# Kernel optimization log

Measured on AMD Instinct MI355X. Metric: run time of the kernel, lower is better.

## Reference

```python
import jax, jax.numpy as jnp
import numpy as np

N_NODES = 50000
N_EDGES = 800000
B, S, D = 512, 200, 128
H = 8


def setup_inputs() -> dict:
    key = jax.random.key(0)
    ks = iter(jax.random.split(key, 64))
    def nrm(shape, scale=0.05):
        return jax.random.normal(next(ks), shape, dtype=jnp.float32) * scale
    inp = {
        'hist_seq': jax.random.randint(next(ks), (B, S), 0, N_NODES, dtype=jnp.int32),
        'hist_answers': jax.random.randint(next(ks), (B, S), 0, 2, dtype=jnp.int32),
        'new_seq': jax.random.randint(next(ks), (B, S), 0, N_NODES, dtype=jnp.int32),
        'edge_index': jax.random.randint(next(ks), (2, N_EDGES), 0, N_NODES, dtype=jnp.int32),
        'node_x': nrm((N_NODES, D)),
        'gcn_w0': nrm((D, D)), 'gcn_b0': jnp.zeros((D,), jnp.float32),
        'gcn_w1': nrm((D, D)), 'gcn_b1': jnp.zeros((D,), jnp.float32),
        'gcn_w2': nrm((D, D)), 'gcn_b2': jnp.zeros((D,), jnp.float32),
        'ln0_g': jnp.ones((D,), jnp.float32), 'ln0_b': jnp.zeros((D,), jnp.float32),
        'ln1_g': jnp.ones((D,), jnp.float32), 'ln1_b': jnp.zeros((D,), jnp.float32),
        'ln2_g': jnp.ones((D,), jnp.float32), 'ln2_b': jnp.zeros((D,), jnp.float32),
        'ln3_g': jnp.ones((D,), jnp.float32), 'ln3_b': jnp.zeros((D,), jnp.float32),
        'corr_emb': nrm((2, D)),
        'lin0_w': nrm((2 * D, D)), 'lin0_b': jnp.zeros((D,), jnp.float32),
        'lin1_w': nrm((D, D)), 'lin2_w': nrm((D, D)), 'lin3_w': nrm((D, D)),
        'lin4_w': nrm((D, 1)), 'lin4_b': jnp.zeros((1,), jnp.float32),
        'pos_emb': nrm((S, D)),
        'mha_wq': nrm((D, D)), 'mha_bq': jnp.zeros((D,), jnp.float32),
        'mha_wk': nrm((D, D)), 'mha_bk': jnp.zeros((D,), jnp.float32),
        'mha_wv': nrm((D, D)), 'mha_bv': jnp.zeros((D,), jnp.float32),
        'mha_wo': nrm((D, D)), 'mha_bo': jnp.zeros((D,), jnp.float32),
        'ffn0_w': nrm((D, D)), 'ffn0_b': jnp.zeros((D,), jnp.float32),
        'ffn1_w': nrm((D, D)), 'ffn1_b': jnp.zeros((D,), jnp.float32),
    }
    return inp


def _layer_norm(x, g, b, eps=1e-5):
    m = jnp.mean(x, axis=-1, keepdims=True)
    v = jnp.var(x, axis=-1, keepdims=True)
    return (x - m) * jax.lax.rsqrt(v + eps) * g + b


def _forward(hist_seq, hist_answers, new_seq, edge_index, node_x,
             gcn_w0, gcn_b0, gcn_w1, gcn_b1, gcn_w2, gcn_b2,
             ln0_g, ln0_b, ln1_g, ln1_b, ln2_g, ln2_b, ln3_g, ln3_b,
             corr_emb, lin0_w, lin0_b, lin1_w, lin2_w, lin3_w, lin4_w, lin4_b,
             pos_emb, mha_wq, mha_bq, mha_wk, mha_bk, mha_wv, mha_bv,
             mha_wo, mha_bo, ffn0_w, ffn0_b, ffn1_w, ffn1_b):
    N = node_x.shape[0]
    loop = jnp.arange(N, dtype=edge_index.dtype)
    src = jnp.concatenate([edge_index[0], loop])  # self-loops as in PyG GCNConv
    dst = jnp.concatenate([edge_index[1], loop])
    deg = jax.ops.segment_sum(jnp.ones_like(dst, dtype=node_x.dtype), dst, num_segments=N)
    dis = jax.lax.rsqrt(deg)  # deg >= 1 (self-loops)
    norm = dis[src] * dis[dst]

    def gcn(x, W, b):
        xw = x @ W
        return jax.ops.segment_sum(norm[:, None] * xw[src], dst, num_segments=N) + b

    x = _layer_norm(jax.nn.relu(gcn(node_x, gcn_w0, gcn_b0)), ln0_g, ln0_b)
    x = _layer_norm(jax.nn.relu(gcn(x, gcn_w1, gcn_b1)), ln1_g, ln1_b)
    x = jax.nn.relu(gcn(x, gcn_w2, gcn_b2))  # last GCN layer: no LN

    # vectorized embedding gathers (the original's per-element loops)
    hist_emb = x[hist_seq]            # [B,S,D]
    new_emb = x[new_seq]              # [B,S,D]
    ans_emb = corr_emb[hist_answers]  # [B,S,D]

    inter = jnp.concatenate([hist_emb, ans_emb], axis=-1) @ lin0_w + lin0_b
    inter = inter + pos_emb[None]  # [B,S,D]

    v = inter @ lin1_w
    k = inter @ lin2_w
    q = new_emb @ lin3_w

    b_, s_, d_ = q.shape
    dh = d_ // H
    qh = (q @ mha_wq + mha_bq).reshape(b_, s_, H, dh)
    kh = (k @ mha_wk + mha_bk).reshape(b_, s_, H, dh)
    vh = (v @ mha_wv + mha_bv).reshape(b_, s_, H, dh)
    scores = jnp.einsum('bqhd,bkhd->bhqk', qh, kh) / jnp.sqrt(jnp.asarray(dh, q.dtype))
    causal = jnp.triu(jnp.ones((s_, s_), dtype=bool), k=1)
    scores = jnp.where(causal[None, None], -jnp.inf, scores)
    attn = jax.nn.softmax(scores, axis=-1)
    ao = jnp.einsum('bhqk,bkhd->bqhd', attn, vh).reshape(b_, s_, d_)
    ao = ao @ mha_wo + mha_bo

    atn = _layer_norm(ao + q, ln2_g, ln2_b)
    ffn = jax.nn.relu(atn @ ffn0_w + ffn0_b) @ ffn1_w + ffn1_b
    out = _layer_norm(ffn + atn, ln3_g, ln3_b)
    pred = (out @ lin4_w + lin4_b)[..., 0]  # squeeze -> [B,S]
    return pred


def reference(hist_seq, hist_answers, new_seq, edge_index, node_x,
              gcn_w0, gcn_b0, gcn_w1, gcn_b1, gcn_w2, gcn_b2,
              ln0_g, ln0_b, ln1_g, ln1_b, ln2_g, ln2_b, ln3_g, ln3_b,
              corr_emb, lin0_w, lin0_b, lin1_w, lin2_w, lin3_w, lin4_w, lin4_b,
              pos_emb, mha_wq, mha_bq, mha_wk, mha_bk, mha_wv, mha_bv,
              mha_wo, mha_bo, ffn0_w, ffn0_b, ffn1_w, ffn1_b):
    return _forward(hist_seq, hist_answers, new_seq, edge_index, node_x,
                    gcn_w0, gcn_b0, gcn_w1, gcn_b1, gcn_w2, gcn_b2,
                    ln0_g, ln0_b, ln1_g, ln1_b, ln2_g, ln2_b, ln3_g, ln3_b,
                    corr_emb, lin0_w, lin0_b, lin1_w, lin2_w, lin3_w, lin4_w, lin4_b,
                    pos_emb, mha_wq, mha_bq, mha_wk, mha_bk, mha_wv, mha_bv,
                    mha_wo, mha_bo, ffn0_w, ffn0_b, ffn1_w, ffn1_b)
```

## Files before the change

### kernel.cpp

```cpp
#include <hip/hip_runtime.h>
#include <math.h>

#define N_NODES 50000
#define N_EDGES 800000
#define B_ 512
#define S_ 200
#define D_ 128
#define BS_ (B_*S_)

typedef unsigned short u16;
typedef unsigned int u32;
using bfrag = __attribute__((ext_vector_type(8))) short;
using f32x4 = __attribute__((ext_vector_type(4))) float;

__device__ __forceinline__ u16 f2bf(float f) {
  u32 u = __float_as_uint(f);
  u32 r = (u + 0x7fffu + ((u >> 16) & 1u)) >> 16;
  return (u16)r;
}
__device__ __forceinline__ float bf2f(u16 v) { return __uint_as_float(((u32)v) << 16); }
__device__ __forceinline__ float bflo(u32 v) { return __uint_as_float(v << 16); }
__device__ __forceinline__ float bfhi(u32 v) { return __uint_as_float(v & 0xffff0000u); }
__device__ __forceinline__ u32 pack2(float a, float b) {
  return (u32)f2bf(a) | ((u32)f2bf(b) << 16);
}
#define MFMA16(a, b, c) __builtin_amdgcn_mfma_f32_16x16x32_bf16((a), (b), (c), 0, 0, 0)

#define STAGE_W(Wsrc) \
  for (int i_ = threadIdx.x; i_ < 2048; i_ += 256) { \
    int c_ = i_ >> 4, kg_ = i_ & 15; \
    *(uint4*)(sW + c_ * 136 + kg_ * 8) = *(const uint4*)((Wsrc) + c_ * 128 + kg_ * 8); \
  }

__global__ void zero_i32_kernel(int* __restrict__ p, int n) {
  int i = blockIdx.x * 256 + threadIdx.x;
  if (i < n) p[i] = 0;
}

__global__ void f2bf8_kernel(const float* __restrict__ in, u16* __restrict__ out, int n8) {
  int i = blockIdx.x * 256 + threadIdx.x;
  if (i >= n8) return;
  float4 a = ((const float4*)in)[i * 2];
  float4 b = ((const float4*)in)[i * 2 + 1];
  uint4 o;
  o.x = pack2(a.x, a.y); o.y = pack2(a.z, a.w);
  o.z = pack2(b.x, b.y); o.w = pack2(b.z, b.w);
  ((uint4*)out)[i] = o;
}

__global__ __launch_bounds__(256) void wprep_kernel(
    const float* __restrict__ gcn_w0, const float* __restrict__ gcn_w1,
    const float* __restrict__ gcn_w2, const float* __restrict__ lin0_w,
    const float* __restrict__ lin3_w, const float* __restrict__ mha_wo,
    const float* __restrict__ ffn0_w, const float* __restrict__ ffn1_w,
    const float* __restrict__ lin1_w, const float* __restrict__ lin2_w,
    const float* __restrict__ mha_wq, const float* __restrict__ mha_wk,
    const float* __restrict__ mha_wv, const float* __restrict__ corr_emb,
    u16* __restrict__ g0T, u16* __restrict__ g1T, u16* __restrict__ g2T,
    u16* __restrict__ l0T, u16* __restrict__ l3T, u16* __restrict__ woT,
    u16* __restrict__ f0T, u16* __restrict__ f1T,
    u16* __restrict__ wqT, u16* __restrict__ wkT, u16* __restrict__ wvT,
    float* __restrict__ c01) {
  int bb = blockIdx.x;
  if (bb < 512) {
    const float* W; u16* D;
    switch (bb >> 6) {
      case 0: W = gcn_w0; D = g0T; break;
      case 1: W = gcn_w1; D = g1T; break;
      case 2: W = gcn_w2; D = g2T; break;
      case 3: W = lin0_w; D = l0T; break;
      case 4: W = lin3_w; D = l3T; break;
      case 5: W = mha_wo; D = woT; break;
      case 6: W = ffn0_w; D = f0T; break;
      default: W = ffn1_w; D = f1T; break;
    }
    int i = (bb & 63) * 256 + threadIdx.x;
    int k = i >> 7, c = i & 127;
    D[c * 128 + k] = f2bf(W[k * 128 + c]);
  } else if (bb < 704) {
    const float* X; const float* Y; u16* D;
    switch ((bb - 512) >> 6) {
      case 0: X = lin3_w; Y = mha_wq; D = wqT; break;
      case 1: X = lin2_w; Y = mha_wk; D = wkT; break;
      default: X = lin1_w; Y = mha_wv; D = wvT; break;
    }
    int i = ((bb - 512) & 63) * 256 + threadIdx.x;
    int k = i >> 7, c = i & 127;
    float acc = 0.f;
    for (int t = 0; t < 128; ++t) acc += X[k * 128 + t] * Y[t * 128 + c];
    D[c * 128 + k] = f2bf(acc);
  } else {
    int idx = threadIdx.x;
    int i = idx >> 7, j = idx & 127;
    float acc = 0.f;
    for (int t = 0; t < 128; ++t)
      acc += corr_emb[i * 128 + t] * lin0_w[128 * 128 + t * 128 + j];
    c01[idx] = acc;
  }
}

__global__ void pc_kernel(const float* __restrict__ lin0_b, const float* __restrict__ pos_emb,
                          const float* __restrict__ c01, float* __restrict__ pc) {
  int i = blockIdx.x * 256 + threadIdx.x;
  int c = i & 127, s = (i >> 7) % S_, a = i / (128 * S_);
  pc[i] = lin0_b[c] + pos_emb[s * 128 + c] + c01[a * 128 + c];
}

__global__ void hist_kernel(const int* __restrict__ dst, int* __restrict__ cnt, int E) {
  int e = blockIdx.x * 256 + threadIdx.x;
  if (e < E) atomicAdd(&cnt[dst[e]], 1);
}

__global__ __launch_bounds__(1024) void scanA_kernel(
    const int* __restrict__ cnt, int* __restrict__ locpref,
    int* __restrict__ btot, float* __restrict__ dis, int N) {
  __shared__ int wsum[16];
  int t = threadIdx.x, lane = t & 63, wid = t >> 6;
  int i = blockIdx.x * 1024 + t;
  int v = (i < N) ? cnt[i] : 0;
  if (i < N) dis[i] = rsqrtf(1.f + (float)v);
  int x = v;
  #pragma unroll
  for (int off = 1; off < 64; off <<= 1) {
    int y = __shfl_up(x, off);
    if (lane >= off) x += y;
  }
  if (lane == 63) wsum[wid] = x;
  __syncthreads();
  if (wid == 0 && lane < 16) {
    int s = wsum[lane];
    #pragma unroll
    for (int off = 1; off < 16; off <<= 1) {
      int y = __shfl_up(s, off);
      if (lane >= off) s += y;
    }
    wsum[lane] = s;
  }
  __syncthreads();
  int woff = (wid > 0) ? wsum[wid - 1] : 0;
  if (i < N) locpref[i] = woff + x - v;
  if (t == 1023) btot[blockIdx.x] = woff + x;
}

__global__ void scanB_kernel(const int* __restrict__ btot, int* __restrict__ boff, int nb) {
  int lane = threadIdx.x;
  int v = (lane < nb) ? btot[lane] : 0;
  int x = v;
  #pragma unroll
  for (int off = 1; off < 64; off <<= 1) {
    int y = __shfl_up(x, off);
    if (lane >= off) x += y;
  }
  if (lane < nb) boff[lane] = x - v;
}

__global__ void scanC_kernel(const int* __restrict__ locpref, const int* __restrict__ boff,
                             int* __restrict__ row_ptr, int* __restrict__ fill, int N) {
  int i = blockIdx.x * 256 + threadIdx.x;
  if (i < N) {
    int r = locpref[i] + boff[i >> 10];
    row_ptr[i] = r; fill[i] = r;
  }
  if (i == 0) row_ptr[N] = N_EDGES;
}

__global__ void scatter_kernel(const int* __restrict__ src, const int* __restrict__ dst,
                               int* __restrict__ fill, int* __restrict__ csr_src, int E) {
  int e = blockIdx.x * 256 + threadIdx.x;
  if (e >= E) return;
  int d = dst[e];
  int pos = atomicAdd(&fill[d], 1);
  csr_src[pos] = src[e];
}

__global__ __launch_bounds__(256) void gemm_bf16_kernel(
    const u16* __restrict__ A, const u16* __restrict__ wT,
    u16* __restrict__ C, int M) {
  __shared__ u16 ldsb[4][16 * 136];
  int t = threadIdx.x;
  int w = t >> 6, l = t & 63, lr = l & 15, lg = l >> 4;
  int r0 = blockIdx.x * 64 + w * 16;

  int row = r0 + lr;
  const u16* Arow = A + (size_t)(row < M ? row : 0) * 128;

  bfrag a[4];
  #pragma unroll
  for (int ks = 0; ks < 4; ++ks) a[ks] = *(const bfrag*)(Arow + ks * 32 + lg * 8);

  f32x4 acc[8];
  #pragma unroll
  for (int ct = 0; ct < 8; ++ct) acc[ct] = (f32x4){0.f, 0.f, 0.f, 0.f};
  #pragma unroll
  for (int ks = 0; ks < 4; ++ks)
    #pragma unroll
    for (int ct = 0; ct < 8; ++ct) {
      bfrag b = *(const bfrag*)(wT + (size_t)(ct * 16 + lr) * 128 + ks * 32 + lg * 8);
      acc[ct] = MFMA16(a[ks], b, acc[ct]);
    }
  #pragma unroll
  for (int ct = 0; ct < 8; ++ct)
    #pragma unroll
    for (int i = 0; i < 4; ++i)
      ldsb[w][(lg * 4 + i) * 136 + ct * 16 + lr] = f2bf(acc[ct][i]);
  #pragma unroll
  for (int j = 0; j < 4; ++j) {
    int c = j * 64 + l;
    int rw = c >> 4, ch = c & 15;
    int r = r0 + rw;
    if (r < M)
      *(uint4*)(C + (size_t)r * 128 + ch * 8) = *(const uint4*)&ldsb[w][rw * 136 + ch * 8];
  }
}

__global__ __launch_bounds__(256) void agg_kernel(
    const u16* __restrict__ xw, const float* __restrict__ dis,
    const int* __restrict__ row_ptr, const int* __restrict__ csr_src,
    const float* __restrict__ bias, const float* __restrict__ lng,
    const float* __restrict__ lnb, u16* __restrict__ out, int N, int doLN) {
  int t = threadIdx.x;
  int n = blockIdx.x * 4 + (t >> 6);
  if (n >= N) return;
  int l = t & 63, cg = l & 15, eg = l >> 4;
  float dn = dis[n];
  float acc[8] = {0.f, 0.f, 0.f, 0.f, 0.f, 0.f, 0.f, 0.f};
  if (eg == 0) {
    uint4 r = *(const uint4*)(xw + (size_t)n * 128 + cg * 8);
    float w = dn * dn;
    acc[0] += w * bflo(r.x); acc[1] += w * bfhi(r.x);
    acc[2] += w * bflo(r.y); acc[3] += w * bfhi(r.y);
    acc[4] += w * bflo(r.z); acc[5] += w * bfhi(r.z);
    acc[6] += w * bflo(r.w); acc[7] += w * bfhi(r.w);
  }
  int e1 = row_ptr[n + 1];
  int e = row_ptr[n] + eg;
  int sn = (e < e1) ? csr_src[e] : -1;
  while (sn >= 0) {
    int s = sn;
    e += 4;
    sn = (e < e1) ? csr_src[e] : -1;
    float w = dis[s] * dn;
    uint4 r = *(const uint4*)(xw + (size_t)s * 128 + cg * 8);
    acc[0] += w * bflo(r.x); acc[1] += w * bfhi(r.x);
    acc[2] += w * bflo(r.y); acc[3] += w * bfhi(r.y);
    acc[4] += w * bflo(r.z); acc[5] += w * bfhi(r.z);
    acc[6] += w * bflo(r.w); acc[7] += w * bfhi(r.w);
  }
  #pragma unroll
  for (int j = 0; j < 8; ++j) {
    acc[j] += __shfl_xor(acc[j], 16);
    acc[j] += __shfl_xor(acc[j], 32);
  }
  int c0 = cg * 8;
  #pragma unroll
  for (int j = 0; j < 8; ++j) acc[j] = fmaxf(acc[j] + bias[c0 + j], 0.f);
  if (doLN) {
    float s1 = 0.f, s2 = 0.f;
    #pragma unroll
    for (int j = 0; j < 8; ++j) { s1 += acc[j]; s2 += acc[j] * acc[j]; }
    #pragma unroll
    for (int off = 1; off < 16; off <<= 1) {
      s1 += __shfl_xor(s1, off);
      s2 += __shfl_xor(s2, off);
    }
    float mean = s1 * (1.f / 128.f);
    float var = s2 * (1.f / 128.f) - mean * mean;
    float inv = rsqrtf(var + 1e-5f);
    #pragma unroll
    for (int j = 0; j < 8; ++j)
      acc[j] = (acc[j] - mean) * inv * lng[c0 + j] + lnb[c0 + j];
  }
  if (eg == 0) {
    uint4 o;
    o.x = pack2(acc[0], acc[1]); o.y = pack2(acc[2], acc[3]);
    o.z = pack2(acc[4], acc[5]); o.w = pack2(acc[6], acc[7]);
    *(uint4*)(out + (size_t)n * 128 + cg * 8) = o;
  }
}

__global__ __launch_bounds__(256) void qkv_kernel(
    const u16* __restrict__ xa, const int* __restrict__ hist,
    const int* __restrict__ ans, const int* __restrict__ nseq,
    const u16* __restrict__ l0T, const float* __restrict__ pc,
    const u16* __restrict__ wkT, const float* __restrict__ bk,
    const u16* __restrict__ wvT, const float* __restrict__ bv,
    const u16* __restrict__ wqT, const float* __restrict__ bq,
    u16* __restrict__ khout, u16* __restrict__ vhout,
    u16* __restrict__ qhout, int nblk) {
  __shared__ u16 sW[128 * 136];
  __shared__ u16 ldsb[4][16 * 136];
  int bb = blockIdx.x;
  int t = threadIdx.x, w = t >> 6, l = t & 63, lr = l & 15, lg = l >> 4;
  f32x4 acc[8];

  if (bb < nblk) {
    int r0 = bb * 64 + w * 16;
    int arow = hist[r0 + lr];
    const u16* Arow = xa + (size_t)arow * 128;
    bfrag a[4];
    #pragma unroll
    for (int ks = 0; ks < 4; ++ks) a[ks] = *(const bfrag*)(Arow + ks * 32 + lg * 8);

    STAGE_W(l0T);
    __syncthreads();
    #pragma unroll
    for (int ct = 0; ct < 8; ++ct) acc[ct] = (f32x4){0.f, 0.f, 0.f, 0.f};
    #pragma unroll
    for (int ks = 0; ks < 4; ++ks)
      #pragma unroll
      for (int ct = 0; ct < 8; ++ct) {
        bfrag b = *(const bfrag*)(sW + (ct * 16 + lr) * 136 + ks * 32 + lg * 8);
        acc[ct] = MFMA16(a[ks], b, acc[ct]);
      }
    int pcoff[4];
    #pragma unroll
    for (int i = 0; i < 4; ++i) {
      int r = r0 + lg * 4 + i;
      pcoff[i] = (ans[r] * S_ + (r % S_)) * 128;
    }
    #pragma unroll
    for (int ct = 0; ct < 8; ++ct) {
      int col = ct * 16 + lr;
      #pragma unroll
      for (int i = 0; i < 4; ++i)
        ldsb[w][(lg * 4 + i) * 136 + col] = f2bf(acc[ct][i] + pc[pcoff[i] + col]);
    }
    bfrag a2[4];
    #pragma unroll
    for (int ks = 0; ks < 4; ++ks)
      a2[ks] = *(const bfrag*)(&ldsb[w][lr * 136 + ks * 32 + lg * 8]);
    __syncthreads();

    STAGE_W(wkT);
    __syncthreads();
    #pragma unroll
    for (int ct = 0; ct < 8; ++ct) acc[ct] = (f32x4){0.f, 0.f, 0.f, 0.f};
    #pragma unroll
    for (int ks = 0; ks < 4; ++ks)
      #pragma unroll
      for (int ct = 0; ct < 8; ++ct) {
        bfrag b = *(const bfrag*)(sW + (ct * 16 + lr) * 136 + ks * 32 + lg * 8);
        acc[ct] = MFMA16(a2[ks], b, acc[ct]);
      }
    #pragma unroll
    for (int ct = 0; ct < 8; ++ct)
      #pragma unroll
      for (int i = 0; i < 4; ++i)
        ldsb[w][(lg * 4 + i) * 136 + ct * 16 + lr] = f2bf(acc[ct][i] + bk[ct * 16 + lr]);
    #pragma unroll
    for (int j = 0; j < 4; ++j) {
      int c = j * 64 + l;
      int head = c >> 5, rw = (c >> 1) & 15, half = c & 1;
      *(uint4*)(khout + ((size_t)head * BS_ + r0 + rw) * 16 + half * 8) =
          *(const uint4*)&ldsb[w][rw * 136 + head * 16 + half * 8];
    }
    __syncthreads();

    STAGE_W(wvT);
    __syncthreads();
    #pragma unroll
    for (int ct = 0; ct < 8; ++ct) acc[ct] = (f32x4){0.f, 0.f, 0.f, 0.f};
    #pragma unroll
    for (int ks = 0; ks < 4; ++ks)
      #pragma unroll
      for (int ct = 0; ct < 8; ++ct) {
        bfrag b = *(const bfrag*)(sW + (ct * 16 + lr) * 136 + ks * 32 + lg * 8);
        acc[ct] = MFMA16(a2[ks], b, acc[ct]);
      }
    #pragma unroll
    for (int ct = 0; ct < 8; ++ct)
      #pragma unroll
      for (int i = 0; i < 4; ++i)
        ldsb[w][(lg * 4 + i) * 136 + ct * 16 + lr] = f2bf(acc[ct][i] + bv[ct * 16 + lr]);
    #pragma unroll
    for (int j = 0; j < 4; ++j) {
      int c = j * 64 + l;
      int head = c >> 5, rw = (c >> 1) & 15, half = c & 1;
      *(uint4*)(vhout + ((size_t)head * BS_ + r0 + rw) * 16 + half * 8) =
          *(const uint4*)&ldsb[w][rw * 136 + head * 16 + half * 8];
    }
  } else {
    int r0 = (bb - nblk) * 64 + w * 16;
    int arow = nseq[r0 + lr];
    const u16* Arow = xa + (size_t)arow * 128;
    bfrag a[4];
    #pragma unroll
    for (int ks = 0; ks < 4; ++ks) a[ks] = *(const bfrag*)(Arow + ks * 32 + lg * 8);

    STAGE_W(wqT);
    __syncthreads();
    #pragma unroll
    for (int ct = 0; ct < 8; ++ct) acc[ct] = (f32x4){0.f, 0.f, 0.f, 0.f};
    #pragma unroll
    for (int ks = 0; ks < 4; ++ks)
      #pragma unroll
      for (int ct = 0; ct < 8; ++ct) {
        bfrag b = *(const bfrag*)(sW + (ct * 16 + lr) * 136 + ks * 32 + lg * 8);
        acc[ct] = MFMA16(a[ks], b, acc[ct]);
      }
    #pragma unroll
    for (int ct = 0; ct < 8; ++ct)
      #pragma unroll
      for (int i = 0; i < 4; ++i)
        ldsb[w][(lg * 4 + i) * 136 + ct * 16 + lr] = f2bf(acc[ct][i] + bq[ct * 16 + lr]);
    #pragma unroll
    for (int j = 0; j < 4; ++j) {
      int c = j * 64 + l;
      int head = c >> 5, rw = (c >> 1) & 15, half = c & 1;
      *(uint4*)(qhout + ((size_t)head * BS_ + r0 + rw) * 16 + half * 8) =
          *(const uint4*)&ldsb[w][rw * 136 + head * 16 + half * 8];
    }
  }
}

__global__ __launch_bounds__(256) void attn_mfma_kernel(
    u16* qh_ao, const u16* __restrict__ kh, const u16* __restrict__ vh) {
  __shared__ u16 Kl[208 * 24];
  __shared__ u16 Vt[16 * 232];
  __shared__ u16 Pl[4 * 16 * 232];
  int b = blockIdx.x >> 3, h = blockIdx.x & 7;
  int t = threadIdx.x;
  size_t base = ((size_t)h * BS_ + (size_t)b * S_) * 16;

  for (int i = t; i < 208 * 2; i += 256) {
    int key = i >> 1, d = (i & 1) * 8;
    uint4 v = make_uint4(0, 0, 0, 0);
    if (key < S_) v = *(const uint4*)(kh + base + (size_t)key * 16 + d);
    *(uint4*)(Kl + key * 24 + d) = v;
  }
  for (int i = t; i < 16 * 232; i += 256) {
    int d = i / 232, key = i - d * 232;
    Vt[d * 232 + key] = (key < S_) ? vh[base + (size_t)key * 16 + d] : (u16)0;
  }
  for (int i = t; i < 4 * 16 * 232 / 2; i += 256) ((u32*)Pl)[i] = 0;
  __syncthreads();

  int w = t >> 6, l = t & 63, lr = l & 15, lg = l >> 4;
  u16* Pw = Pl + w * 16 * 232;
  const f32x4 zero4 = {0.f, 0.f, 0.f, 0.f};

  for (int qi = w; qi < 13; qi += 4) {
    bfrag aq = (bfrag){0, 0, 0, 0, 0, 0, 0, 0};
    int qrow = qi * 16 + lr;
    if (lg < 2 && qrow < S_)
      aq = *(const bfrag*)(qh_ao + base + (size_t)qrow * 16 + lg * 8);
    float rsum[4] = {0.f, 0.f, 0.f, 0.f};
    for (int kj = 0; kj <= qi; ++kj) {
      bfrag bk = (bfrag){0, 0, 0, 0, 0, 0, 0, 0};
      if (lg < 2) bk = *(const bfrag*)(Kl + (kj * 16 + lr) * 24 + lg * 8);
      f32x4 sc = MFMA16(aq, bk, zero4);
      #pragma unroll
      for (int i = 0; i < 4; ++i) {
        int q = qi * 16 + lg * 4 + i, key = kj * 16 + lr;
        float p = 0.f;
        if (key <= q && q < S_) p = __expf(sc[i] * 0.25f);
        rsum[i] += p;
        Pw[(lg * 4 + i) * 232 + key] = f2bf(p);
      }
    }
    #pragma unroll
    for (int i = 0; i < 4; ++i) {
      rsum[i] += __shfl_xor(rsum[i], 1);
      rsum[i] += __shfl_xor(rsum[i], 2);
      rsum[i] += __shfl_xor(rsum[i], 4);
      rsum[i] += __shfl_xor(rsum[i], 8);
    }
    f32x4 o = zero4;
    #pragma unroll
    for (int kt = 0; kt < 7; ++kt) {
      bfrag ap = *(const bfrag*)(Pw + lr * 232 + kt * 32 + lg * 8);
      bfrag bv = *(const bfrag*)(Vt + lr * 232 + kt * 32 + lg * 8);
      o = MFMA16(ap, bv, o);
    }
    #pragma unroll
    for (int i = 0; i < 4; ++i) {
      int q = qi * 16 + lg * 4 + i;
      if (q < S_) qh_ao[base + (size_t)q * 16 + lr] = f2bf(o[i] / rsum[i]);
    }
  }
}

__global__ __launch_bounds__(256) void out_kernel(
    const u16* __restrict__ ao, const u16* __restrict__ xa,
    const int* __restrict__ nseq,
    const u16* __restrict__ woT, const float* __restrict__ bo,
    const u16* __restrict__ l3T,
    const float* __restrict__ g2, const float* __restrict__ b2,
    const u16* __restrict__ f0T, const float* __restrict__ b0f,
    const u16* __restrict__ f1T, const float* __restrict__ b1f,
    const float* __restrict__ g3, const float* __restrict__ b3,
    const float* __restrict__ w4, const float* __restrict__ b4,
    float* __restrict__ pred) {
  __shared__ u16 sW[128 * 136];
  __shared__ u16 ldsb[4][16 * 136];
  int t = threadIdx.x, w = t >> 6, l = t & 63, lr = l & 15, lg = l >> 4;
  int r0 = blockIdx.x * 64 + w * 16;

  bfrag a_ao[4], a_xa[4];
  #pragma unroll
  for (int ks = 0; ks < 4; ++ks) {
    int head = ks * 2 + (lg >> 1);
    int d0 = (lg & 1) * 8;
    a_ao[ks] = *(const bfrag*)(ao + ((size_t)head * BS_ + r0 + lr) * 16 + d0);
  }
  {
    int arow = nseq[r0 + lr];
    const u16* Arow = xa + (size_t)arow * 128;
    #pragma unroll
    for (int ks = 0; ks < 4; ++ks) a_xa[ks] = *(const bfrag*)(Arow + ks * 32 + lg * 8);
  }

  f32x4 acc[8];
  #pragma unroll
  for (int ct = 0; ct < 8; ++ct) acc[ct] = (f32x4){0.f, 0.f, 0.f, 0.f};

  STAGE_W(woT);
  __syncthreads();
  #pragma unroll
  for (int ks = 0; ks < 4; ++ks)
    #pragma unroll
    for (int ct = 0; ct < 8; ++ct) {
      bfrag b = *(const bfrag*)(sW + (ct * 16 + lr) * 136 + ks * 32 + lg * 8);
      acc[ct] = MFMA16(a_ao[ks], b, acc[ct]);
    }
  __syncthreads();

  STAGE_W(l3T);
  __syncthreads();
  #pragma unroll
  for (int ks = 0; ks < 4; ++ks)
    #pragma unroll
    for (int ct = 0; ct < 8; ++ct) {
      bfrag b = *(const bfrag*)(sW + (ct * 16 + lr) * 136 + ks * 32 + lg * 8);
      acc[ct] = MFMA16(a_xa[ks], b, acc[ct]);
    }
  __syncthreads();

  #pragma unroll
  for (int ct = 0; ct < 8; ++ct) {
    float bcol = bo[ct * 16 + lr];
    #pragma unroll
    for (int i = 0; i < 4; ++i) acc[ct][i] += bcol;
  }
  bfrag a2[4];
  {
    float s1[4] = {0, 0, 0, 0}, s2[4] = {0, 0, 0, 0};
    #pragma unroll
    for (int ct = 0; ct < 8; ++ct)
      #pragma unroll
      for (int i = 0; i < 4; ++i) {
        s1[i] += acc[ct][i];
        s2[i] += acc[ct][i] * acc[ct][i];
      }
    #pragma unroll
    for (int i = 0; i < 4; ++i) {
      s1[i] += __shfl_xor(s1[i], 1); s2[i] += __shfl_xor(s2[i], 1);
      s1[i] += __shfl_xor(s1[i], 2); s2[i] += __shfl_xor(s2[i], 2);
      s1[i] += __shfl_xor(s1[i], 4); s2[i] += __shfl_xor(s2[i], 4);
      s1[i] += __shfl_xor(s1[i], 8); s2[i] += __shfl_xor(s2[i], 8);
    }
    float mean[4], inv[4];
    #pragma unroll
    for (int i = 0; i < 4; ++i) {
      mean[i] = s1[i] * (1.f / 128.f);
      float var = s2[i] * (1.f / 128.f) - mean[i] * mean[i];
      inv[i] = rsqrtf(var + 1e-5f);
    }
    #pragma unroll
    for (int ct = 0; ct < 8; ++ct) {
      int col = ct * 16 + lr;
      float gc = g2[col], bc = b2[col];
      #pragma unroll
      for (int i = 0; i < 4; ++i) {
        acc[ct][i] = (acc[ct][i] - mean[i]) * inv[i] * gc + bc;
        ldsb[w][(lg * 4 + i) * 136 + col] = f2bf(acc[ct][i]);
      }
    }
    #pragma unroll
    for (int ks = 0; ks < 4; ++ks)
      a2[ks] = *(const bfrag*)(&ldsb[w][lr * 136 + ks * 32 + lg * 8]);
  }

  STAGE_W(f0T);
  __syncthreads();
  f32x4 acc2[8];
  #pragma unroll
  for (int ct = 0; ct < 8; ++ct) acc2[ct] = (f32x4){0.f, 0.f, 0.f, 0.f};
  #pragma unroll
  for (int ks = 0; ks < 4; ++ks)
    #pragma unroll
    for (int ct = 0; ct < 8; ++ct) {
      bfrag b = *(const bfrag*)(sW + (ct * 16 + lr) * 136 + ks * 32 + lg * 8);
      acc2[ct] = MFMA16(a2[ks], b, acc2[ct]);
    }
  #pragma unroll
  for (int ct = 0; ct < 8; ++ct) {
    int col = ct * 16 + lr;
    float bcol = b0f[col];
    #pragma unroll
    for (int i = 0; i < 4; ++i)
      ldsb[w][(lg * 4 + i) * 136 + col] = f2bf(fmaxf(acc2[ct][i] + bcol, 0.f));
  }
  #pragma unroll
  for (int ks = 0; ks < 4; ++ks)
    a2[ks] = *(const bfrag*)(&ldsb[w][lr * 136 + ks * 32 + lg * 8]);
  __syncthreads();

  STAGE_W(f1T);
  __syncthreads();
  #pragma unroll
  for (int ct = 0; ct < 8; ++ct) acc2[ct] = (f32x4){0.f, 0.f, 0.f, 0.f};
  #pragma unroll
  for (int ks = 0; ks < 4; ++ks)
    #pragma unroll
    for (int ct = 0; ct < 8; ++ct) {
      bfrag b = *(const bfrag*)(sW + (ct * 16 + lr) * 136 + ks * 32 + lg * 8);
      acc2[ct] = MFMA16(a2[ks], b, acc2[ct]);
    }
  #pragma unroll
  for (int ct = 0; ct < 8; ++ct) {
    int col = ct * 16 + lr;
    float bcol = b1f[col];
    #pragma unroll
    for (int i = 0; i < 4; ++i) acc2[ct][i] += bcol + acc[ct][i];
  }
  {
    float s1[4] = {0, 0, 0, 0}, s2[4] = {0, 0, 0, 0};
    #pragma unroll
    for (int ct = 0; ct < 8; ++ct)
      #pragma unroll
      for (int i = 0; i < 4; ++i) {
        s1[i] += acc2[ct][i];
        s2[i] += acc2[ct][i] * acc2[ct][i];
      }
    #pragma unroll
    for (int i = 0; i < 4; ++i) {
      s1[i] += __shfl_xor(s1[i], 1); s2[i] += __shfl_xor(s2[i], 1);
      s1[i] += __shfl_xor(s1[i], 2); s2[i] += __shfl_xor(s2[i], 2);
      s1[i] += __shfl_xor(s1[i], 4); s2[i] += __shfl_xor(s2[i], 4);
      s1[i] += __shfl_xor(s1[i], 8); s2[i] += __shfl_xor(s2[i], 8);
    }
    float p[4] = {0, 0, 0, 0};
    #pragma unroll
    for (int i = 0; i < 4; ++i) {
      float mean = s1[i] * (1.f / 128.f);
      float var = s2[i] * (1.f / 128.f) - mean * mean;
      float inv = rsqrtf(var + 1e-5f);
      #pragma unroll
      for (int ct = 0; ct < 8; ++ct) {
        int col = ct * 16 + lr;
        p[i] += ((acc2[ct][i] - mean) * inv * g3[col] + b3[col]) * w4[col];
      }
    }
    #pragma unroll
    for (int i = 0; i < 4; ++i) {
      p[i] += __shfl_xor(p[i], 1);
      p[i] += __shfl_xor(p[i], 2);
      p[i] += __shfl_xor(p[i], 4);
      p[i] += __shfl_xor(p[i], 8);
    }
    if (lr == 0) {
      float bias4 = b4[0];
      #pragma unroll
      for (int i = 0; i < 4; ++i) pred[r0 + lg * 4 + i] = p[i] + bias4;
    }
  }
}

extern "C" void kernel_launch(void* const* d_in, const int* in_sizes, int n_in,
                              void* d_out, int out_size, void* d_ws, size_t ws_size,
                              hipStream_t stream) {
  const int* hist_seq = (const int*)d_in[0];
  const int* hist_ans = (const int*)d_in[1];
  const int* new_seq = (const int*)d_in[2];
  const int* edge_index = (const int*)d_in[3];
  const float* node_x = (const float*)d_in[4];
  const float* gcn_w0 = (const float*)d_in[5];
  const float* gcn_b0 = (const float*)d_in[6];
  const float* gcn_w1 = (const float*)d_in[7];
  const float* gcn_b1 = (const float*)d_in[8];
  const float* gcn_w2 = (const float*)d_in[9];
  const float* gcn_b2 = (const float*)d_in[10];
  const float* ln0_g = (const float*)d_in[11];
  const float* ln0_b = (const float*)d_in[12];
  const float* ln1_g = (const float*)d_in[13];
  const float* ln1_b = (const float*)d_in[14];
  const float* ln2_g = (const float*)d_in[15];
  const float* ln2_b = (const float*)d_in[16];
  const float* ln3_g = (const float*)d_in[17];
  const float* ln3_b = (const float*)d_in[18];
  const float* corr_emb = (const float*)d_in[19];
  const float* lin0_w = (const float*)d_in[20];
  const float* lin0_b = (const float*)d_in[21];
  const float* lin1_w = (const float*)d_in[22];
  const float* lin2_w = (const float*)d_in[23];
  const float* lin3_w = (const float*)d_in[24];
  const float* lin4_w = (const float*)d_in[25];
  const float* lin4_b = (const float*)d_in[26];
  const float* pos_emb = (const float*)d_in[27];
  const float* mha_wq = (const float*)d_in[28];
  const float* mha_bq = (const float*)d_in[29];
  const float* mha_wk = (const float*)d_in[30];
  const float* mha_bk = (const float*)d_in[31];
  const float* mha_wv = (const float*)d_in[32];
  const float* mha_bv = (const float*)d_in[33];
  const float* mha_wo = (const float*)d_in[34];
  const float* mha_bo = (const float*)d_in[35];
  const float* ffn0_w = (const float*)d_in[36];
  const float* ffn0_b = (const float*)d_in[37];
  const float* ffn1_w = (const float*)d_in[38];
  const float* ffn1_b = (const float*)d_in[39];
  (void)in_sizes; (void)n_in; (void)out_size;

  char* ws = (char*)d_ws;
  size_t off = 0;
  auto alloc = [&](size_t bytes) -> void* {
    void* p = ws + off;
    off += (bytes + 255) & ~(size_t)255;
    return p;
  };
  int* cnt = (int*)alloc((size_t)N_NODES * 4);
  int* row_ptr = (int*)alloc((size_t)(N_NODES + 1) * 4);
  int* fill = (int*)alloc((size_t)N_NODES * 4);
  int* locpref = (int*)alloc((size_t)N_NODES * 4);
  int* btot = (int*)alloc(64 * 4);
  int* boff = (int*)alloc(64 * 4);
  float* dis = (float*)alloc((size_t)N_NODES * 4);
  int* csr_src = (int*)alloc((size_t)N_EDGES * 4);
  const size_t WB = 128 * 128 * 2;
  u16* g0T = (u16*)alloc(WB);
  u16* g1T = (u16*)alloc(WB);
  u16* g2T = (u16*)alloc(WB);
  u16* l0T = (u16*)alloc(WB);
  u16* l3T = (u16*)alloc(WB);
  u16* woT = (u16*)alloc(WB);
  u16* f0T = (u16*)alloc(WB);
  u16* f1T = (u16*)alloc(WB);
  u16* wqT = (u16*)alloc(WB);
  u16* wkT = (u16*)alloc(WB);
  u16* wvT = (u16*)alloc(WB);
  float* c01 = (float*)alloc(2 * 128 * 4);
  float* pc = (float*)alloc((size_t)2 * S_ * 128 * 4);
  u16* xa = (u16*)alloc((size_t)N_NODES * 128 * 2);
  const size_t CB = (size_t)BS_ * 128 * 2;
  size_t RB = off;
  u16* bufQ = (u16*)(ws + RB);
  u16* bufK = (u16*)(ws + RB + CB);
  u16* bufV = (u16*)(ws + RB + 2 * CB);
  u16* xb = bufQ;
  u16* xw = bufQ + (size_t)N_NODES * 128;
  size_t need = RB + 3 * CB;
  if (ws_size < need) return;

  int nb = (N_NODES + 1023) / 1024;
  zero_i32_kernel<<<(N_NODES + 255) / 256, 256, 0, stream>>>(cnt, N_NODES);
  hist_kernel<<<(N_EDGES + 255) / 256, 256, 0, stream>>>(edge_index + N_EDGES, cnt, N_EDGES);
  scanA_kernel<<<nb, 1024, 0, stream>>>(cnt, locpref, btot, dis, N_NODES);
  scanB_kernel<<<1, 64, 0, stream>>>(btot, boff, nb);
  scanC_kernel<<<(N_NODES + 255) / 256, 256, 0, stream>>>(locpref, boff, row_ptr, fill, N_NODES);
  scatter_kernel<<<(N_EDGES + 255) / 256, 256, 0, stream>>>(edge_index, edge_index + N_EDGES,
                                                            fill, csr_src, N_EDGES);
  wprep_kernel<<<705, 256, 0, stream>>>(gcn_w0, gcn_w1, gcn_w2, lin0_w, lin3_w, mha_wo,
                                        ffn0_w, ffn1_w, lin1_w, lin2_w, mha_wq, mha_wk,
                                        mha_wv, corr_emb, g0T, g1T, g2T, l0T, l3T, woT,
                                        f0T, f1T, wqT, wkT, wvT, c01);
  pc_kernel<<<(2 * S_ * 128 + 255) / 256, 256, 0, stream>>>(lin0_b, pos_emb, c01, pc);
  f2bf8_kernel<<<(N_NODES * 16 + 255) / 256, 256, 0, stream>>>(node_x, xb, N_NODES * 16);

  int gN = (N_NODES + 63) / 64;
  int aN = (N_NODES + 3) / 4;

  gemm_bf16_kernel<<<gN, 256, 0, stream>>>(xb, g0T, xw, N_NODES);
  agg_kernel<<<aN, 256, 0, stream>>>(xw, dis, row_ptr, csr_src, gcn_b0, ln0_g, ln0_b, xa, N_NODES, 1);
  gemm_bf16_kernel<<<gN, 256, 0, stream>>>(xa, g1T, xw, N_NODES);
  agg_kernel<<<aN, 256, 0, stream>>>(xw, dis, row_ptr, csr_src, gcn_b1, ln1_g, ln1_b, xa, N_NODES, 1);
  gemm_bf16_kernel<<<gN, 256, 0, stream>>>(xa, g2T, xw, N_NODES);
  agg_kernel<<<aN, 256, 0, stream>>>(xw, dis, row_ptr, csr_src, gcn_b2, nullptr, nullptr, xa, N_NODES, 0);

  int gT = BS_ / 64;
  qkv_kernel<<<2 * gT, 256, 0, stream>>>(xa, hist_seq, hist_ans, new_seq,
                                         l0T, pc, wkT, mha_bk, wvT, mha_bv,
                                         wqT, mha_bq, bufK, bufV, bufQ, gT);
  attn_mfma_kernel<<<B_ * 8, 256, 0, stream>>>(bufQ, bufK, bufV);
  out_kernel<<<gT, 256, 0, stream>>>(bufQ, xa, new_seq, woT, mha_bo, l3T,
                                     ln2_g, ln2_b, f0T, ffn0_b, f1T, ffn1_b,
                                     ln3_g, ln3_b, lin4_w, lin4_b, (float*)d_out);
}
```

Measured before the change: 450.2 us.

## Balance causal attention tiles across warps and skip masked work

The causal attention kernel now gives each warp a hand-picked, load-balanced set of query tiles instead of a round-robin split. Off-diagonal key tiles are computed without masks, and only the diagonal tile is masked. The P·V loop runs only over key blocks that can be non-zero. The softmax scale is folded into the Q projection, the bf16 conversion switches to cheaper round-half-up instead of round-to-nearest-even, and the P row stride is shortened. These remove exp/mask work on masked entries, wasted MFMAs and warp imbalance, at the cost of slightly different rounding and a hardcoded schedule tied to 13 tiles.

```diff
diff --git a/kernel.cpp b/kernel.cpp
--- a/kernel.cpp
+++ b/kernel.cpp
@@ -7,6 +7,7 @@
 #define S_ 200
 #define D_ 128
 #define BS_ (B_*S_)
+#define PSTR 228
 
 typedef unsigned short u16;
 typedef unsigned int u32;
@@ -14,9 +15,7 @@
 using f32x4 = __attribute__((ext_vector_type(4))) float;
 
 __device__ __forceinline__ u16 f2bf(float f) {
-  u32 u = __float_as_uint(f);
-  u32 r = (u + 0x7fffu + ((u >> 16) & 1u)) >> 16;
-  return (u16)r;
+  return (u16)((__float_as_uint(f) + 0x8000u) >> 16);
 }
 __device__ __forceinline__ float bf2f(u16 v) { return __uint_as_float(((u32)v) << 16); }
 __device__ __forceinline__ float bflo(u32 v) { return __uint_as_float(v << 16); }
@@ -402,7 +401,8 @@
     for (int ct = 0; ct < 8; ++ct)
       #pragma unroll
       for (int i = 0; i < 4; ++i)
-        ldsb[w][(lg * 4 + i) * 136 + ct * 16 + lr] = f2bf(acc[ct][i] + bq[ct * 16 + lr]);
+        ldsb[w][(lg * 4 + i) * 136 + ct * 16 + lr] =
+            f2bf((acc[ct][i] + bq[ct * 16 + lr]) * 0.25f);
     #pragma unroll
     for (int j = 0; j < 4; ++j) {
       int c = j * 64 + l;
@@ -417,7 +417,7 @@
     u16* qh_ao, const u16* __restrict__ kh, const u16* __restrict__ vh) {
   __shared__ u16 Kl[208 * 24];
   __shared__ u16 Vt[16 * 232];
-  __shared__ u16 Pl[4 * 16 * 232];
+  __shared__ u16 Pl[4 * 16 * PSTR];
   int b = blockIdx.x >> 3, h = blockIdx.x & 7;
   int t = threadIdx.x;
   size_t base = ((size_t)h * BS_ + (size_t)b * S_) * 16;
@@ -432,30 +432,45 @@
     int d = i / 232, key = i - d * 232;
     Vt[d * 232 + key] = (key < S_) ? vh[base + (size_t)key * 16 + d] : (u16)0;
   }
-  for (int i = t; i < 4 * 16 * 232 / 2; i += 256) ((u32*)Pl)[i] = 0;
+  for (int i = t; i < 4 * 16 * PSTR / 2; i += 256) ((u32*)Pl)[i] = 0;
   __syncthreads();
 
   int w = t >> 6, l = t & 63, lr = l & 15, lg = l >> 4;
-  u16* Pw = Pl + w * 16 * 232;
+  u16* Pw = Pl + w * 16 * PSTR;
   const f32x4 zero4 = {0.f, 0.f, 0.f, 0.f};
-
-  for (int qi = w; qi < 13; qi += 4) {
+  u32 qpack = (w == 0) ? 0xFC71u : (w == 1) ? 0xFB80u : (w == 2) ? 0xFA92u : 0x6543u;
+  int qlocal = lg * 4;
+
+  for (int s = 0; s < 4; ++s) {
+    int qi = (qpack >> (4 * s)) & 15;
+    if (qi == 15) break;
     bfrag aq = (bfrag){0, 0, 0, 0, 0, 0, 0, 0};
     int qrow = qi * 16 + lr;
     if (lg < 2 && qrow < S_)
       aq = *(const bfrag*)(qh_ao + base + (size_t)qrow * 16 + lg * 8);
     float rsum[4] = {0.f, 0.f, 0.f, 0.f};
-    for (int kj = 0; kj <= qi; ++kj) {
+    for (int kj = 0; kj < qi; ++kj) {
       bfrag bk = (bfrag){0, 0, 0, 0, 0, 0, 0, 0};
       if (lg < 2) bk = *(const bfrag*)(Kl + (kj * 16 + lr) * 24 + lg * 8);
       f32x4 sc = MFMA16(aq, bk, zero4);
       #pragma unroll
       for (int i = 0; i < 4; ++i) {
-        int q = qi * 16 + lg * 4 + i, key = kj * 16 + lr;
-        float p = 0.f;
-        if (key <= q && q < S_) p = __expf(sc[i] * 0.25f);
+        float p = __expf(sc[i]);
         rsum[i] += p;
-        Pw[(lg * 4 + i) * 232 + key] = f2bf(p);
+        Pw[(qlocal + i) * PSTR + kj * 16 + lr] = f2bf(p);
+      }
+    }
+    {
+      bfrag bk = (bfrag){0, 0, 0, 0, 0, 0, 0, 0};
+      if (lg < 2) bk = *(const bfrag*)(Kl + (qi * 16 + lr) * 24 + lg * 8);
+      f32x4 sc = MFMA16(aq, bk, zero4);
+      #pragma unroll
+      for (int i = 0; i < 4; ++i) {
+        if (lr <= qlocal + i) {
+          float p = __expf(sc[i]);
+          rsum[i] += p;
+          Pw[(qlocal + i) * PSTR + qi * 16 + lr] = f2bf(p);
+        }
       }
     }
     #pragma unroll
@@ -466,15 +481,15 @@
       rsum[i] += __shfl_xor(rsum[i], 8);
     }
     f32x4 o = zero4;
-    #pragma unroll
-    for (int kt = 0; kt < 7; ++kt) {
-      bfrag ap = *(const bfrag*)(Pw + lr * 232 + kt * 32 + lg * 8);
+    int ktmax = (qi + 2) >> 1;
+    for (int kt = 0; kt < ktmax; ++kt) {
+      bfrag ap = *(const bfrag*)(Pw + lr * PSTR + kt * 32 + lg * 8);
       bfrag bv = *(const bfrag*)(Vt + lr * 232 + kt * 32 + lg * 8);
       o = MFMA16(ap, bv, o);
     }
     #pragma unroll
     for (int i = 0; i < 4; ++i) {
-      int q = qi * 16 + lg * 4 + i;
+      int q = qi * 16 + qlocal + i;
       if (q < S_) qh_ao[base + (size_t)q * 16 + lr] = f2bf(o[i] / rsum[i]);
     }
   }
```

Measured after the change: 447.1 us. No clear change (-0.7%).
